# Optimization experiments

Measured on AMD Instinct MI355X. Metric: run time of the kernel, lower is better.

## Reference

```python
import math
import itertools
import jax, jax.numpy as jnp
import numpy as np

SEQ_LEN = 16
D_IN = 2048
TSS = 3          # temporal_set_size
D_OUT = 1128
PE_SCALE = 0.1
N_SUPPORT = 5
N_QUERIES = 1
LN_EPS = 1e-5


def _pos_enc(seq_len, d_model):
    pos = np.arange(seq_len, dtype=np.float32)[:, None]
    div = np.exp(np.arange(0, d_model, 2, dtype=np.float32) * -(math.log(10000.0) / d_model))
    pe = np.zeros((seq_len, d_model), dtype=np.float32)
    pe[:, 0::2] = np.sin(pos * div) * PE_SCALE
    pe[:, 1::2] = np.cos(pos * div) * PE_SCALE
    return jnp.asarray(pe)


def _tuples(seq_len, k):
    return np.asarray(list(itertools.combinations(range(seq_len), k)), dtype=np.int32)  # [T, k]


def setup_inputs() -> dict:
    key = jax.random.key(0)
    ks = jax.random.split(key, 8)
    return {
        "support_set": jax.random.normal(ks[0], (N_SUPPORT, SEQ_LEN, D_IN), jnp.float32),
        "queries": jax.random.normal(ks[1], (N_QUERIES, SEQ_LEN, D_IN), jnp.float32),
        "support_labels": jnp.arange(N_SUPPORT, dtype=jnp.int64),
        "wk": jax.random.normal(ks[2], (D_OUT, D_IN * TSS), jnp.float32) * 0.02,
        "bk": jax.random.normal(ks[3], (D_OUT,), jnp.float32) * 0.02,
        "wv": jax.random.normal(ks[4], (D_OUT, D_IN * TSS), jnp.float32) * 0.02,
        "bv": jax.random.normal(ks[5], (D_OUT,), jnp.float32) * 0.02,
        "gamma": jnp.ones((D_OUT,), jnp.float32),
        "beta": jnp.zeros((D_OUT,), jnp.float32),
    }


def _layer_norm(x, gamma, beta):
    mu = jnp.mean(x, axis=-1, keepdims=True)
    var = jnp.mean(jnp.square(x - mu), axis=-1, keepdims=True)
    return (x - mu) * jax.lax.rsqrt(var + LN_EPS) * gamma + beta


def reference(support_set, queries, support_labels, wk, bk, wv, bv, gamma, beta):
    tup = _tuples(SEQ_LEN, TSS)                      # [T, 3] static
    T = tup.shape[0]                                 # tuples_len = C(16,3) = 560
    pe = _pos_enc(SEQ_LEN, D_IN)                     # [S, D_IN]

    s = support_set + pe                             # [5, S, D_IN]
    q = queries + pe                                 # [1, S, D_IN]

    # gather frame tuples and flatten: [n, T, 3*D_IN]
    s_t = s[:, tup, :].reshape(N_SUPPORT, T, TSS * D_IN)
    q_t = q[:, tup, :].reshape(N_QUERIES, T, TSS * D_IN)

    s_ks = _layer_norm(s_t @ wk.T + bk, gamma, beta)  # [5, T, D_OUT]
    q_ks = _layer_norm(q_t @ wk.T + bk, gamma, beta)  # [1, T, D_OUT]
    s_vs = s_t @ wv.T + bv                            # [5, T, D_OUT]
    q_vs = q_t @ wv.T + bv                            # [1, T, D_OUT]

    # _extract_class_indices returns the label value itself -> direct row gather
    ck = s_ks[support_labels]                         # [C, T, D_OUT]
    cv = s_vs[support_labels]                         # [C, T, D_OUT]

    scores = jnp.einsum('qtd,csd->cqts', q_ks, ck) / math.sqrt(D_OUT)  # [C, Q, T, T]
    attn = jax.nn.softmax(scores, axis=-1)            # softmax over support tuples
    proto = jnp.einsum('cqts,csd->cqtd', attn, cv)    # [C, Q, T, D_OUT]

    diff = q_vs[None] - proto                         # [C, Q, T, D_OUT]
    dist = -jnp.sum(diff * diff, axis=(-2, -1)) / T   # [C, Q]
    logits = dist.T                                   # [Q, C]
    return logits
```

## Files before the change

kernel.cpp:

```cpp
#include <hip/hip_runtime.h>
#include <hip/hip_bf16.h>

#define SEQ 16
#define DIN 2048
#define TSS 3
#define DOUT 1128
#define DPAD 1152
#define NT 560
#define NTPAD 576
#define NSEQ 6
#define NCOL 6768
#define W1CNT 6930432

typedef __attribute__((ext_vector_type(4))) float f32x4;
typedef __attribute__((ext_vector_type(8))) short bf16x8;

__device__ __forceinline__ float bf2f(unsigned short h) {
    union { unsigned int u; float f; } c; c.u = ((unsigned int)h) << 16; return c.f;
}
__device__ __forceinline__ unsigned short f2bf(float f) {
    union { float f; unsigned int u; } c; c.f = f;
    unsigned int lsb = (c.u >> 16) & 1;
    c.u += 0x7fffu + lsb;
    return (unsigned short)(c.u >> 16);
}
__device__ __forceinline__ float loadf(const void* p, size_t i, int f32m) {
    return f32m ? ((const float*)p)[i] : bf2f(((const unsigned short*)p)[i]);
}
__device__ __forceinline__ int probe_f32(const void* gamma) {
    return (((const unsigned int*)gamma)[0] == 0x3F800000u) ? 1 : 0;
}
__device__ __forceinline__ int probe_i64(const void* labels) {
    return (((const long long*)labels)[1] == 1LL) ? 1 : 0;
}
__device__ __forceinline__ int get_label(const void* p, int c, int is64) {
    long long v = is64 ? ((const long long*)p)[c] : (long long)((const int*)p)[c];
    if (v < 0) v = 0; if (v > 4) v = 4;
    return (int)v;
}


__global__ __launch_bounds__(256) void k_build_wx(
        const void* __restrict__ sup, const void* __restrict__ qry,
        const void* __restrict__ wk, const void* __restrict__ wv,
        const void* __restrict__ gamma,
        unsigned short* __restrict__ XF, unsigned short* __restrict__ WbF) {
    int f32m = probe_f32(gamma);
    if (blockIdx.x < 96) {
        int c8 = blockIdx.x * 256 + threadIdx.x;
        int idx512 = c8 >> 6;
        int rowgrp = idx512 >> 6, kt = idx512 & 63;
        int sub = c8 & 63;
        int r15 = sub & 15;
        int row = rowgrp * 16 + r15;
        int f = row & 15, n = row >> 4;
        int k = kt * 32 + (sub >> 4) * 8;
        bf16x8 ov;
#pragma unroll
        for (int j = 0; j < 8; ++j) {
            int d = k + j;
            float v = (n < 5) ? loadf(sup, (size_t)row * DIN + d, f32m)
                              : loadf(qry, (size_t)f * DIN + d, f32m);
            int m2 = d & ~1;
            float div = __expf(-(float)m2 * (9.210340371976184f / 2048.0f));
            float ang = (float)f * div;
            float pe = ((d & 1) ? __cosf(ang) : __sinf(ang)) * 0.1f;
            ov[j] = (short)f2bf(v + pe);
        }
        *(bf16x8*)(XF + (size_t)c8 * 8) = ov;
    } else {
        size_t c8 = (size_t)(blockIdx.x - 96) * 256 + threadIdx.x;
        size_t idx512 = c8 >> 6;
        int colgrp = (int)(idx512 >> 6);
        int kt = (int)(idx512 & 63);
        int sub = (int)(c8 & 63);
        int col = colgrp * 16 + (sub & 15);
        int k = kt * 32 + (sub >> 4) * 8;
        int which = col / 3384; int rem = col - which * 3384;
        int seg = rem / DOUT;   int o = rem - seg * DOUT;
        const void* src = which ? wv : wk;
        size_t si = (size_t)o * (TSS * DIN) + (size_t)seg * DIN + k;
        if (f32m) {
            f32x4 w0 = *(const f32x4*)((const float*)src + si);
            f32x4 w1 = *(const f32x4*)((const float*)src + si + 4);
            bf16x8 ov;
#pragma unroll
            for (int j = 0; j < 4; ++j) {
                ov[j]     = (short)f2bf(w0[j]);
                ov[4 + j] = (short)f2bf(w1[j]);
            }
            *(bf16x8*)(WbF + c8 * 8) = ov;
        } else {
            *(bf16x8*)(WbF + c8 * 8) = *(const bf16x8*)((const unsigned short*)src + si);
        }
    }
}

__global__ __launch_bounds__(256) void k_proj(
        const unsigned short* __restrict__ XF, const unsigned short* __restrict__ WbF,
        unsigned short* __restrict__ Pb) {
    int tn = blockIdx.x;
    int tid = threadIdx.x;
    int w = tid >> 6, lane = tid & 63;
    int c16 = lane & 15, quad = lane >> 4;
    int cg0 = tn * 2;
    int cg1 = (tn * 2 + 1 > 422) ? 422 : tn * 2 + 1;
    const unsigned short* bF0 = WbF + ((size_t)cg0 << 15) + lane * 8;
    const unsigned short* bF1 = WbF + ((size_t)cg1 << 15) + lane * 8;
    const unsigned short* aF  = XF + lane * 8;

    f32x4 acc[6][2];
#pragma unroll
    for (int m = 0; m < 6; ++m)
#pragma unroll
        for (int ch = 0; ch < 2; ++ch) acc[m][ch] = (f32x4){0.f, 0.f, 0.f, 0.f};

    int ktb = w * 16;
#pragma unroll 2
    for (int kt = ktb; kt < ktb + 16; ++kt) {
        bf16x8 b0 = *(const bf16x8*)(bF0 + ((size_t)kt << 9));
        bf16x8 b1 = *(const bf16x8*)(bF1 + ((size_t)kt << 9));
#pragma unroll
        for (int m = 0; m < 6; ++m) {
            bf16x8 a = *(const bf16x8*)(aF + ((size_t)(m * 64 + kt) << 9));
            acc[m][0] = __builtin_amdgcn_mfma_f32_16x16x32_bf16(a, b0, acc[m][0], 0, 0, 0);
            acc[m][1] = __builtin_amdgcn_mfma_f32_16x16x32_bf16(a, b1, acc[m][1], 0, 0, 0);
        }
    }
    __shared__ float red[3 * 12 * 64 * 4];
    if (w > 0) {
#pragma unroll
        for (int m = 0; m < 6; ++m)
#pragma unroll
            for (int ch = 0; ch < 2; ++ch)
#pragma unroll
                for (int r = 0; r < 4; ++r)
                    red[(((w - 1) * 12 + m * 2 + ch) * 64 + lane) * 4 + r] = acc[m][ch][r];
    }
    __syncthreads();
    if (w == 0) {
#pragma unroll
        for (int m = 0; m < 6; ++m)
#pragma unroll
            for (int ch = 0; ch < 2; ++ch) {
                int t = m * 2 + ch;
#pragma unroll
                for (int r = 0; r < 4; ++r) {
                    float s = acc[m][ch][r]
                            + red[((0 * 12 + t) * 64 + lane) * 4 + r]
                            + red[((1 * 12 + t) * 64 + lane) * 4 + r]
                            + red[((2 * 12 + t) * 64 + lane) * 4 + r];
                    int row = m * 16 + quad * 4 + r;
                    int col = tn * 32 + ch * 16 + c16;
                    if (col < NCOL) Pb[(size_t)row * NCOL + col] = f2bf(s);
                }
            }
    }
}

__global__ __launch_bounds__(256) void k_combine_ln(
        const unsigned short* __restrict__ Pb,
        const void* __restrict__ bk, const void* __restrict__ bv,
        const void* __restrict__ gamma, const void* __restrict__ beta,
        unsigned short* __restrict__ ksF, unsigned short* __restrict__ vs) {
    int n = blockIdx.x / NT, t = blockIdx.x % NT;
    int f32m = probe_f32(gamma);
    int idx = t, fi, fj, fk;
    for (fi = 0;; ++fi) { int c2 = (15 - fi) * (14 - fi) / 2; if (idx < c2) break; idx -= c2; }
    for (fj = fi + 1;; ++fj) { int c1 = 15 - fj; if (idx < c1) break; idx -= c1; }
    fk = fj + 1 + idx;
    size_t ri = (size_t)(n * 16 + fi) * NCOL;
    size_t rj = (size_t)(n * 16 + fj) * NCOL;
    size_t rk = (size_t)(n * 16 + fk) * NCOL;

    float kv[5], vv[5];
    float s = 0.f, s2 = 0.f;
#pragma unroll
    for (int it = 0; it < 5; ++it) {
        int o = threadIdx.x + it * 256;
        kv[it] = 0.f; vv[it] = 0.f;
        if (o < DOUT) {
            float a = bf2f(Pb[ri + o]) + bf2f(Pb[rj + DOUT + o])
                    + bf2f(Pb[rk + 2 * DOUT + o]) + loadf(bk, o, f32m);
            float b = bf2f(Pb[ri + 3 * DOUT + o]) + bf2f(Pb[rj + 4 * DOUT + o])
                    + bf2f(Pb[rk + 5 * DOUT + o]) + loadf(bv, o, f32m);
            kv[it] = a; vv[it] = b;
            s += a; s2 += a * a;
        }
    }
    __shared__ float red[8];
#pragma unroll
    for (int off = 32; off; off >>= 1) { s += __shfl_down(s, off); s2 += __shfl_down(s2, off); }
    int wid = threadIdx.x >> 6;
    if ((threadIdx.x & 63) == 0) { red[wid] = s; red[4 + wid] = s2; }
    __syncthreads();
    s = red[0] + red[1] + red[2] + red[3];
    s2 = red[4] + red[5] + red[6] + red[7];
    float mu = s / (float)DOUT;
    float var = s2 / (float)DOUT - mu * mu;
    float rstd = rsqrtf(var + 1e-5f);

    size_t ntbase = ((size_t)(n * 36 + (t >> 4)) * 36) * 512 + (size_t)(t & 15) * 8;
    size_t vbase = ((size_t)n * NT + t) * DPAD;
#pragma unroll
    for (int it = 0; it < 5; ++it) {
        int o = threadIdx.x + it * 256;
        if (o < DPAD) {
            float kres = 0.f;
            if (o < DOUT)
                kres = (kv[it] - mu) * rstd * loadf(gamma, o, f32m) + loadf(beta, o, f32m);
            ksF[ntbase + ((size_t)(o >> 5) << 9) + (((o >> 3) & 3) << 7) + (o & 7)] =
                (o < DOUT) ? f2bf(kres) : 0;
            vs[vbase + o] = (o < DOUT) ? f2bf(vv[it]) : 0;
        }
    }
}

__global__ __launch_bounds__(256) void k_transpose(
        const unsigned short* __restrict__ vs, unsigned short* __restrict__ vsTF) {
    int b = blockIdx.x;
    int tt = b % 18; b /= 18; int ot = b % 36; int n = b / 36;
    int t0 = tt * 32, o0 = ot * 32;
    int tx = threadIdx.x & 31, ty = threadIdx.x >> 5;
    __shared__ unsigned short tile[32][33];
#pragma unroll
    for (int i = 0; i < 4; ++i) {
        int t = t0 + ty + 8 * i;
        tile[ty + 8 * i][tx] = (t < NT) ? vs[((size_t)n * NT + t) * DPAD + o0 + tx] : 0;
    }
    __syncthreads();
#pragma unroll
    for (int i = 0; i < 4; ++i) {
        int r = ty + 8 * i;
        size_t addr = ((size_t)(n * 72 + ot * 2 + (r >> 4)) * 18 + tt) * 512
                    + (size_t)((tx >> 3) * 16 + (r & 15)) * 8 + (tx & 7);
        vsTF[addr] = tile[tx][r];
    }
}

__global__ __launch_bounds__(256) void k_scores(
        const unsigned short* __restrict__ ksF, const void* __restrict__ labels,
        float* __restrict__ scores) {
    int b = blockIdx.x;
    int c = b % 5; int rest = b / 5;
    int tm = rest / 9, tn = rest % 9;
    int tid = threadIdx.x;
    int w = tid >> 6, lane = tid & 63;
    int c16 = lane & 15, quad = lane >> 4;
    int lab = get_label(labels, c, probe_i64(labels));
    const unsigned short* aF[4];
    const unsigned short* bF[4];
#pragma unroll
    for (int i = 0; i < 4; ++i) {
        aF[i] = ksF + (((size_t)(5 * 36 + tm * 4 + i) * 36) << 9) + lane * 8;
        bF[i] = ksF + (((size_t)(lab * 36 + tn * 4 + i) * 36) << 9) + lane * 8;
    }
    f32x4 acc[4][4];
#pragma unroll
    for (int i = 0; i < 4; ++i)
#pragma unroll
        for (int j = 0; j < 4; ++j) acc[i][j] = (f32x4){0.f, 0.f, 0.f, 0.f};

    int ktb = w * 9;
#pragma unroll 2
    for (int kt = ktb; kt < ktb + 9; ++kt) {
        bf16x8 a[4], bv4[4];
#pragma unroll
        for (int i = 0; i < 4; ++i) a[i]   = *(const bf16x8*)(aF[i] + ((size_t)kt << 9));
#pragma unroll
        for (int j = 0; j < 4; ++j) bv4[j] = *(const bf16x8*)(bF[j] + ((size_t)kt << 9));
#pragma unroll
        for (int i = 0; i < 4; ++i)
#pragma unroll
            for (int j = 0; j < 4; ++j)
                acc[i][j] = __builtin_amdgcn_mfma_f32_16x16x32_bf16(a[i], bv4[j], acc[i][j], 0, 0, 0);
    }
    __shared__ float red[3 * 16 * 64 * 4];
    if (w > 0) {
#pragma unroll
        for (int i = 0; i < 4; ++i)
#pragma unroll
            for (int j = 0; j < 4; ++j)
#pragma unroll
                for (int r = 0; r < 4; ++r)
                    red[(((w - 1) * 16 + i * 4 + j) * 64 + lane) * 4 + r] = acc[i][j][r];
    }
    __syncthreads();
    if (w == 0) {
        const float scale = 0.029774540f;
#pragma unroll
        for (int i = 0; i < 4; ++i)
#pragma unroll
            for (int j = 0; j < 4; ++j) {
                int t = i * 4 + j;
#pragma unroll
                for (int r = 0; r < 4; ++r) {
                    float s = acc[i][j][r]
                            + red[((0 * 16 + t) * 64 + lane) * 4 + r]
                            + red[((1 * 16 + t) * 64 + lane) * 4 + r]
                            + red[((2 * 16 + t) * 64 + lane) * 4 + r];
                    int tq = tm * 64 + i * 16 + quad * 4 + r;
                    int ts = tn * 64 + j * 16 + c16;
                    scores[((size_t)c * NTPAD + tq) * NTPAD + ts] = s * scale;
                }
            }
    }
}

__global__ __launch_bounds__(256) void k_softmax(
        const float* __restrict__ scores, unsigned short* __restrict__ attnF) {
    int row = blockIdx.x * 4 + (threadIdx.x >> 6);
    int lane = threadIdx.x & 63;
    int c = row / NTPAD, tq = row % NTPAD;
    unsigned short* dstc = attnF + ((size_t)(c * 36 + (tq >> 4)) * 18) * 512 + (size_t)(tq & 15) * 8;
    if (tq >= NT) {
#pragma unroll
        for (int i = 0; i < 9; ++i) {
            int ts = lane + i * 64;
            dstc[((ts >> 5) << 9) + ((ts >> 3) & 3) * 128 + (ts & 7)] = 0;
        }
        return;
    }
    const float* src = scores + (size_t)row * NTPAD;
    float vals[9];
    float m = -1e30f;
#pragma unroll
    for (int i = 0; i < 9; ++i) {
        int idx = lane + i * 64;
        vals[i] = (idx < NT) ? src[idx] : -1e30f;
        m = fmaxf(m, vals[i]);
    }
#pragma unroll
    for (int off = 32; off; off >>= 1) m = fmaxf(m, __shfl_xor(m, off));
    float s = 0.f;
#pragma unroll
    for (int i = 0; i < 9; ++i) {
        int idx = lane + i * 64;
        vals[i] = (idx < NT) ? __expf(vals[i] - m) : 0.f;
        s += vals[i];
    }
#pragma unroll
    for (int off = 32; off; off >>= 1) s += __shfl_xor(s, off);
    float inv = 1.f / s;
#pragma unroll
    for (int i = 0; i < 9; ++i) {
        int ts = lane + i * 64;
        dstc[((ts >> 5) << 9) + ((ts >> 3) & 3) * 128 + (ts & 7)] =
            (ts < NT) ? f2bf(vals[i] * inv) : 0;
    }
}

__global__ __launch_bounds__(128) void k_proto_dist(
        const unsigned short* __restrict__ attnF, const unsigned short* __restrict__ vs,
        const unsigned short* __restrict__ vsTF,
        const void* __restrict__ labels, float* __restrict__ parts) {
    int b = blockIdx.x;
    int c = b / 162; int rest = b % 162;
    int tm = rest / 18, tn = rest % 18;
    int tid = threadIdx.x;
    int w = tid >> 6, lane = tid & 63;
    int c16 = lane & 15, quad = lane >> 4;
    int lab = get_label(labels, c, probe_i64(labels));
    const unsigned short* aF = attnF + ((size_t)(c * 36 + tm * 4) * 18) * 512 + lane * 8;
    const unsigned short* bF = vsTF + ((size_t)(lab * 72 + tn * 4) * 18) * 512 + lane * 8;
    f32x4 acc[4][4];
#pragma unroll
    for (int i = 0; i < 4; ++i)
#pragma unroll
        for (int j = 0; j < 4; ++j) acc[i][j] = (f32x4){0.f, 0.f, 0.f, 0.f};

    int ktb = w * 9;
#pragma unroll 2
    for (int kt = ktb; kt < ktb + 9; ++kt) {
        bf16x8 a[4], bv4[4];
#pragma unroll
        for (int i = 0; i < 4; ++i) a[i]   = *(const bf16x8*)(aF + ((size_t)(i * 18 + kt) << 9));
#pragma unroll
        for (int j = 0; j < 4; ++j) bv4[j] = *(const bf16x8*)(bF + ((size_t)(j * 18 + kt) << 9));
#pragma unroll
        for (int i = 0; i < 4; ++i)
#pragma unroll
            for (int j = 0; j < 4; ++j)
                acc[i][j] = __builtin_amdgcn_mfma_f32_16x16x32_bf16(a[i], bv4[j], acc[i][j], 0, 0, 0);
    }
    __shared__ float red[16 * 64 * 4];
    if (w == 1) {
#pragma unroll
        for (int i = 0; i < 4; ++i)
#pragma unroll
            for (int j = 0; j < 4; ++j)
#pragma unroll
                for (int r = 0; r < 4; ++r)
                    red[((i * 4 + j) * 64 + lane) * 4 + r] = acc[i][j][r];
    }
    __syncthreads();
    if (w == 0) {
        const unsigned short* qv = vs + (size_t)5 * NT * DPAD;
        float part = 0.f;
#pragma unroll
        for (int i = 0; i < 4; ++i)
#pragma unroll
            for (int j = 0; j < 4; ++j) {
                int t = i * 4 + j;
#pragma unroll
                for (int r = 0; r < 4; ++r) {
                    float s = acc[i][j][r] + red[(t * 64 + lane) * 4 + r];
                    int tq = tm * 64 + i * 16 + quad * 4 + r;
                    int o  = tn * 64 + j * 16 + c16;
                    if (tq < NT && o < DOUT) {
                        float d = bf2f(qv[(size_t)tq * DPAD + o]) - s;
                        part += d * d;
                    }
                }
            }
#pragma unroll
        for (int off = 32; off; off >>= 1) part += __shfl_down(part, off);
        if (lane == 0) parts[blockIdx.x] = part;
    }
}

__global__ __launch_bounds__(320) void k_final(const float* __restrict__ parts,
                                               const void* __restrict__ gamma,
                                               void* __restrict__ out) {
    int c = threadIdx.x >> 6;
    int lane = threadIdx.x & 63;
    float s = 0.f;
    for (int i = lane; i < 162; i += 64) s += parts[c * 162 + i];
#pragma unroll
    for (int off = 32; off; off >>= 1) s += __shfl_down(s, off);
    if (lane == 0) {
        float v = -s * (1.0f / (float)NT);
        if (probe_f32(gamma)) ((float*)out)[c] = v;
        else ((unsigned short*)out)[c] = f2bf(v);
    }
}

extern "C" void kernel_launch(void* const* d_in, const int* in_sizes, int n_in,
                              void* d_out, int out_size, void* d_ws, size_t ws_size,
                              hipStream_t stream) {
    const void* sup   = d_in[0];
    const void* qry   = d_in[1];
    const void* labs  = d_in[2];
    const void* wk    = d_in[3];
    const void* bk    = d_in[4];
    const void* wv    = d_in[5];
    const void* bv    = d_in[6];
    const void* gamma = d_in[7];
    const void* beta  = d_in[8];

    char* ws = (char*)d_ws;
    unsigned short* XF     = (unsigned short*)(ws + 256);
    unsigned short* Pb     = (unsigned short*)(ws + 393472);
    float*          parts  = (float*)(ws + 2992384);
    unsigned short* WbF    = (unsigned short*)(ws + 5604352);
    unsigned short* ksF    = (unsigned short*)(ws + 33326080);
    unsigned short* vsb    = (unsigned short*)(ws + 41288704);
    float*          scores = (float*)(ws + 49030144);
    unsigned short* attnF  = (unsigned short*)(ws + 55665664);
    unsigned short* vsTF   = (unsigned short*)(ws + 58983424);

    k_build_wx  <<<96 + 6768, 256, 0, stream>>>(sup, qry, wk, wv, gamma, XF, WbF);
    k_proj      <<<212, 256, 0, stream>>>(XF, WbF, Pb);
    k_combine_ln<<<NSEQ * NT, 256, 0, stream>>>(Pb, bk, bv, gamma, beta, ksF, vsb);
    k_transpose <<<5 * 36 * 18, 256, 0, stream>>>(vsb, vsTF);
    k_scores    <<<405, 256, 0, stream>>>(ksF, labs, scores);
    k_softmax   <<<720, 256, 0, stream>>>(scores, attnF);
    k_proto_dist<<<810, 128, 0, stream>>>(attnF, vsb, vsTF, labs, parts);
    k_final     <<<1, 320, 0, stream>>>(parts, gamma, d_out);
}
```

Measured before the change: 189.2 us.

## Fuse weight bf16 conversion into projection GEMM, dropping the staging buffer

The weight conversion pass, which wrote a bf16 MFMA-fragment copy of wk/wv (about 28MB) to workspace, is removed. The projection kernel now reads the fp32 weights directly and converts them to bf16 in registers before each MFMA. Each block now handles one 16-column group instead of two, so the grid doubles to 423 blocks. This removes one full write and read of the weights at the cost of strided fp32 weight loads and conversion work inside the GEMM loop.

```diff
diff --git a/kernel.cpp b/kernel.cpp
--- a/kernel.cpp
+++ b/kernel.cpp
@@ -10,7 +10,6 @@
 #define NTPAD 576
 #define NSEQ 6
 #define NCOL 6768
-#define W1CNT 6930432
 
 typedef __attribute__((ext_vector_type(4))) float f32x4;
 typedef __attribute__((ext_vector_type(8))) short bf16x8;
@@ -40,121 +39,109 @@
 }
 
 
-__global__ __launch_bounds__(256) void k_build_wx(
+__global__ __launch_bounds__(256) void k_build_x(
         const void* __restrict__ sup, const void* __restrict__ qry,
+        const void* __restrict__ gamma,
+        unsigned short* __restrict__ XF) {
+    int f32m = probe_f32(gamma);
+    int c8 = blockIdx.x * 256 + threadIdx.x;
+    int idx512 = c8 >> 6;
+    int rowgrp = idx512 >> 6, kt = idx512 & 63;
+    int sub = c8 & 63;
+    int r15 = sub & 15;
+    int row = rowgrp * 16 + r15;
+    int f = row & 15, n = row >> 4;
+    int k = kt * 32 + (sub >> 4) * 8;
+    bf16x8 ov;
+#pragma unroll
+    for (int j = 0; j < 8; ++j) {
+        int d = k + j;
+        float v = (n < 5) ? loadf(sup, (size_t)row * DIN + d, f32m)
+                          : loadf(qry, (size_t)f * DIN + d, f32m);
+        int m2 = d & ~1;
+        float div = __expf(-(float)m2 * (9.210340371976184f / 2048.0f));
+        float ang = (float)f * div;
+        float pe = ((d & 1) ? __cosf(ang) : __sinf(ang)) * 0.1f;
+        ov[j] = (short)f2bf(v + pe);
+    }
+    *(bf16x8*)(XF + (size_t)c8 * 8) = ov;
+}
+
+__global__ __launch_bounds__(256) void k_proj(
+        const unsigned short* __restrict__ XF,
         const void* __restrict__ wk, const void* __restrict__ wv,
         const void* __restrict__ gamma,
-        unsigned short* __restrict__ XF, unsigned short* __restrict__ WbF) {
+        unsigned short* __restrict__ Pb) {
     int f32m = probe_f32(gamma);
-    if (blockIdx.x < 96) {
-        int c8 = blockIdx.x * 256 + threadIdx.x;
-        int idx512 = c8 >> 6;
-        int rowgrp = idx512 >> 6, kt = idx512 & 63;
-        int sub = c8 & 63;
-        int r15 = sub & 15;
-        int row = rowgrp * 16 + r15;
-        int f = row & 15, n = row >> 4;
-        int k = kt * 32 + (sub >> 4) * 8;
-        bf16x8 ov;
-#pragma unroll
-        for (int j = 0; j < 8; ++j) {
-            int d = k + j;
-            float v = (n < 5) ? loadf(sup, (size_t)row * DIN + d, f32m)
-                              : loadf(qry, (size_t)f * DIN + d, f32m);
-            int m2 = d & ~1;
-            float div = __expf(-(float)m2 * (9.210340371976184f / 2048.0f));
-            float ang = (float)f * div;
-            float pe = ((d & 1) ? __cosf(ang) : __sinf(ang)) * 0.1f;
-            ov[j] = (short)f2bf(v + pe);
-        }
-        *(bf16x8*)(XF + (size_t)c8 * 8) = ov;
-    } else {
-        size_t c8 = (size_t)(blockIdx.x - 96) * 256 + threadIdx.x;
-        size_t idx512 = c8 >> 6;
-        int colgrp = (int)(idx512 >> 6);
-        int kt = (int)(idx512 & 63);
-        int sub = (int)(c8 & 63);
-        int col = colgrp * 16 + (sub & 15);
-        int k = kt * 32 + (sub >> 4) * 8;
-        int which = col / 3384; int rem = col - which * 3384;
-        int seg = rem / DOUT;   int o = rem - seg * DOUT;
-        const void* src = which ? wv : wk;
-        size_t si = (size_t)o * (TSS * DIN) + (size_t)seg * DIN + k;
-        if (f32m) {
-            f32x4 w0 = *(const f32x4*)((const float*)src + si);
-            f32x4 w1 = *(const f32x4*)((const float*)src + si + 4);
-            bf16x8 ov;
-#pragma unroll
-            for (int j = 0; j < 4; ++j) {
-                ov[j]     = (short)f2bf(w0[j]);
-                ov[4 + j] = (short)f2bf(w1[j]);
-            }
-            *(bf16x8*)(WbF + c8 * 8) = ov;
-        } else {
-            *(bf16x8*)(WbF + c8 * 8) = *(const bf16x8*)((const unsigned short*)src + si);
-        }
-    }
-}
-
-__global__ __launch_bounds__(256) void k_proj(
-        const unsigned short* __restrict__ XF, const unsigned short* __restrict__ WbF,
-        unsigned short* __restrict__ Pb) {
-    int tn = blockIdx.x;
+    int cg = blockIdx.x;
     int tid = threadIdx.x;
     int w = tid >> 6, lane = tid & 63;
     int c16 = lane & 15, quad = lane >> 4;
-    int cg0 = tn * 2;
-    int cg1 = (tn * 2 + 1 > 422) ? 422 : tn * 2 + 1;
-    const unsigned short* bF0 = WbF + ((size_t)cg0 << 15) + lane * 8;
-    const unsigned short* bF1 = WbF + ((size_t)cg1 << 15) + lane * 8;
-    const unsigned short* aF  = XF + lane * 8;
-
-    f32x4 acc[6][2];
-#pragma unroll
-    for (int m = 0; m < 6; ++m)
-#pragma unroll
-        for (int ch = 0; ch < 2; ++ch) acc[m][ch] = (f32x4){0.f, 0.f, 0.f, 0.f};
+    int col = cg * 16 + c16;
+    int which = col / 3384; int rem = col - which * 3384;
+    int seg = rem / DOUT;   int o = rem - seg * DOUT;
+    const void* src = which ? wv : wk;
+    size_t sbase = (size_t)o * (TSS * DIN) + (size_t)seg * DIN + (size_t)quad * 8;
+    const unsigned short* aF = XF + lane * 8;
+
+    f32x4 acc[6];
+#pragma unroll
+    for (int m = 0; m < 6; ++m) acc[m] = (f32x4){0.f, 0.f, 0.f, 0.f};
 
     int ktb = w * 16;
+    if (f32m) {
+        const float* s32 = (const float*)src + sbase;
 #pragma unroll 2
-    for (int kt = ktb; kt < ktb + 16; ++kt) {
-        bf16x8 b0 = *(const bf16x8*)(bF0 + ((size_t)kt << 9));
-        bf16x8 b1 = *(const bf16x8*)(bF1 + ((size_t)kt << 9));
-#pragma unroll
-        for (int m = 0; m < 6; ++m) {
-            bf16x8 a = *(const bf16x8*)(aF + ((size_t)(m * 64 + kt) << 9));
-            acc[m][0] = __builtin_amdgcn_mfma_f32_16x16x32_bf16(a, b0, acc[m][0], 0, 0, 0);
-            acc[m][1] = __builtin_amdgcn_mfma_f32_16x16x32_bf16(a, b1, acc[m][1], 0, 0, 0);
-        }
-    }
-    __shared__ float red[3 * 12 * 64 * 4];
+        for (int kt = ktb; kt < ktb + 16; ++kt) {
+            f32x4 w0 = *(const f32x4*)(s32 + (size_t)kt * 32);
+            f32x4 w1 = *(const f32x4*)(s32 + (size_t)kt * 32 + 4);
+            bf16x8 b;
+#pragma unroll
+            for (int j = 0; j < 4; ++j) {
+                b[j]     = (short)f2bf(w0[j]);
+                b[4 + j] = (short)f2bf(w1[j]);
+            }
+#pragma unroll
+            for (int m = 0; m < 6; ++m) {
+                bf16x8 a = *(const bf16x8*)(aF + ((size_t)(m * 64 + kt) << 9));
+                acc[m] = __builtin_amdgcn_mfma_f32_16x16x32_bf16(a, b, acc[m], 0, 0, 0);
+            }
+        }
+    } else {
+        const unsigned short* s16 = (const unsigned short*)src + sbase;
+#pragma unroll 2
+        for (int kt = ktb; kt < ktb + 16; ++kt) {
+            bf16x8 b = *(const bf16x8*)(s16 + (size_t)kt * 32);
+#pragma unroll
+            for (int m = 0; m < 6; ++m) {
+                bf16x8 a = *(const bf16x8*)(aF + ((size_t)(m * 64 + kt) << 9));
+                acc[m] = __builtin_amdgcn_mfma_f32_16x16x32_bf16(a, b, acc[m], 0, 0, 0);
+            }
+        }
+    }
+
+    __shared__ float red[3 * 6 * 64 * 4];
     if (w > 0) {
 #pragma unroll
         for (int m = 0; m < 6; ++m)
 #pragma unroll
-            for (int ch = 0; ch < 2; ++ch)
-#pragma unroll
-                for (int r = 0; r < 4; ++r)
-                    red[(((w - 1) * 12 + m * 2 + ch) * 64 + lane) * 4 + r] = acc[m][ch][r];
+            for (int r = 0; r < 4; ++r)
+                red[(((w - 1) * 6 + m) * 64 + lane) * 4 + r] = acc[m][r];
     }
     __syncthreads();
     if (w == 0) {
 #pragma unroll
-        for (int m = 0; m < 6; ++m)
-#pragma unroll
-            for (int ch = 0; ch < 2; ++ch) {
-                int t = m * 2 + ch;
-#pragma unroll
-                for (int r = 0; r < 4; ++r) {
-                    float s = acc[m][ch][r]
-                            + red[((0 * 12 + t) * 64 + lane) * 4 + r]
-                            + red[((1 * 12 + t) * 64 + lane) * 4 + r]
-                            + red[((2 * 12 + t) * 64 + lane) * 4 + r];
-                    int row = m * 16 + quad * 4 + r;
-                    int col = tn * 32 + ch * 16 + c16;
-                    if (col < NCOL) Pb[(size_t)row * NCOL + col] = f2bf(s);
-                }
-            }
+        for (int m = 0; m < 6; ++m) {
+#pragma unroll
+            for (int r = 0; r < 4; ++r) {
+                float s = acc[m][r]
+                        + red[((0 * 6 + m) * 64 + lane) * 4 + r]
+                        + red[((1 * 6 + m) * 64 + lane) * 4 + r]
+                        + red[((2 * 6 + m) * 64 + lane) * 4 + r];
+                int row = m * 16 + quad * 4 + r;
+                Pb[(size_t)row * NCOL + col] = f2bf(s);
+            }
+        }
     }
 }
 
@@ -452,15 +439,14 @@
     unsigned short* XF     = (unsigned short*)(ws + 256);
     unsigned short* Pb     = (unsigned short*)(ws + 393472);
     float*          parts  = (float*)(ws + 2992384);
-    unsigned short* WbF    = (unsigned short*)(ws + 5604352);
     unsigned short* ksF    = (unsigned short*)(ws + 33326080);
     unsigned short* vsb    = (unsigned short*)(ws + 41288704);
     float*          scores = (float*)(ws + 49030144);
     unsigned short* attnF  = (unsigned short*)(ws + 55665664);
     unsigned short* vsTF   = (unsigned short*)(ws + 58983424);
 
-    k_build_wx  <<<96 + 6768, 256, 0, stream>>>(sup, qry, wk, wv, gamma, XF, WbF);
-    k_proj      <<<212, 256, 0, stream>>>(XF, WbF, Pb);
+    k_build_x   <<<96, 256, 0, stream>>>(sup, qry, gamma, XF);
+    k_proj      <<<423, 256, 0, stream>>>(XF, wk, wv, gamma, Pb);
     k_combine_ln<<<NSEQ * NT, 256, 0, stream>>>(Pb, bk, bv, gamma, beta, ksF, vsb);
     k_transpose <<<5 * 36 * 18, 256, 0, stream>>>(vsb, vsTF);
     k_scores    <<<405, 256, 0, stream>>>(ksF, labs, scores);
```

After: 185.9 us. Within noise of the previous version (-1.8%).
